# Performance work log

Hardware: AMD Instinct MI355X
Metric: run time of the kernel (lower is better)

Reference implementation:

```python
import jax, jax.numpy as jnp
import numpy as np

MAX_SX = 10  # max_shiftx
MAX_SY = 10  # max_shifty
STD_EPS = 1e-9


def setup_inputs() -> dict:
    key = jax.random.key(0)
    x = jax.random.normal(key, (8, 32, 128, 128), dtype=jnp.float32)
    return {"x": x}


def _cross_correlation(x):
    b, c, h, w = x.shape
    n = h * w
    # _standartize: zero-mean, divide by (unbiased std * sqrt(h*w)); std<eps -> inf -> 0
    xc = x - jnp.mean(x, axis=(2, 3), keepdims=True)
    std = jnp.std(xc, axis=(2, 3), keepdims=True, ddof=1)
    std = jnp.where(std < STD_EPS, jnp.inf, std)
    xs = xc / (std * jnp.sqrt(jnp.asarray(n, x.dtype)))
    # FFT-based circular cross-correlation for all ordered pairs (i, j>=i)
    Xf = jnp.fft.fft2(xs)  # [b, c, h, w] complex
    ii, jj = np.triu_indices(c)  # row-major: (0,0),(0,1),...,(0,c-1),(1,1),... matches the loop order
    cross = Xf[:, ii] * jnp.conj(Xf[:, jj])  # [b, P, h, w], P = c*(c+1)//2
    cc = jnp.real(jnp.fft.ifft2(cross))
    # The [[br, bl], [tr, tl]] corner concat == roll by (sy, sx) then take leading window
    cc = jnp.roll(cc, (MAX_SY, MAX_SX), axis=(2, 3))
    return cc[:, :, : 2 * MAX_SY + 1, : 2 * MAX_SX + 1]  # [b, P, 2sy+1, 2sx+1]


def reference(x):
    return _cross_correlation(x)
```

## Files before the change

### kernel.cpp

```cpp
#include <hip/hip_runtime.h>
#include <hip/hip_bf16.h>

typedef __attribute__((ext_vector_type(4))) unsigned int uint4v;
typedef __attribute__((ext_vector_type(8))) short short8;
typedef __attribute__((ext_vector_type(16))) float floatx16;

#define NROW 148
#define ROWB (20*512)
#define BB   ((size_t)NROW*ROWB)
#define STATS_OFF ((size_t)8*BB)
#define LDS_A_ROWS 38
#define LDS_BYTES (LDS_A_ROWS*2048 + 32*2048)

__device__ __forceinline__ unsigned short f2b(float f){
  unsigned int u = __float_as_uint(f);
  return (unsigned short)((u + 0x7fffu + ((u >> 16) & 1u)) >> 16);
}

__device__ __forceinline__ void gload_lds16(const void* g, void* l){
  __builtin_amdgcn_global_load_lds((const __attribute__((address_space(1))) unsigned int*)g,
                                   (__attribute__((address_space(3))) unsigned int*)l, 16, 0, 0);
}

__global__ __launch_bounds__(256) void k_stat(const float* __restrict__ x,
                                              float* __restrict__ stats){
  int bid = blockIdx.x;
  int t = threadIdx.x;
  const float* xc = x + ((size_t)bid << 14);
  float s = 0.f, ss = 0.f;
  #pragma unroll 4
  for (int k = 0; k < 64; ++k){
    float v = xc[t + (k << 8)];
    s += v; ss += v*v;
  }
  #pragma unroll
  for (int m = 32; m >= 1; m >>= 1){
    s  += __shfl_xor(s, m);
    ss += __shfl_xor(ss, m);
  }
  __shared__ float rs[4], rss[4];
  int wv = t >> 6, l = t & 63;
  if (l == 0){ rs[wv] = s; rss[wv] = ss; }
  __syncthreads();
  if (t == 0){
    float S  = rs[0]+rs[1]+rs[2]+rs[3];
    float SS = rss[0]+rss[1]+rss[2]+rss[3];
    float mean = S * (1.f/16384.f);
    float var  = (SS - S*mean) * (1.f/16383.f);
    float sd = sqrtf(fmaxf(var, 0.f));
    stats[bid*2]   = mean;
    stats[bid*2+1] = (sd < 1e-9f) ? 0.f : 1.f/(sd*128.f);
  }
}

__global__ __launch_bounds__(512) void k_pack(const float* __restrict__ x,
                                              const float* __restrict__ stats,
                                              unsigned char* __restrict__ pad){
  __shared__ float rowbuf[32*129];
  int bid = blockIdx.x;
  int b = bid & 7, rg = bid >> 3;
  int t = threadIdx.x;
  int ch = t >> 4, xq = t & 15;
  float mean  = stats[(b*32 + ch)*2];
  float scale = stats[(b*32 + ch)*2 + 1];
  const float* xc = x + ((size_t)(b*32 + ch) << 14);
  for (int rr = 0; rr < 4; ++rr){
    int r = rg*4 + rr;
    int sy = (r + 118) & 127;
    const float* src = xc + (sy << 7) + (xq << 3);
    float4 v0 = *(const float4*)src;
    float4 v1 = *(const float4*)(src + 4);
    float* rb = rowbuf + ch*129 + (xq << 3);
    rb[0] = (v0.x-mean)*scale; rb[1] = (v0.y-mean)*scale;
    rb[2] = (v0.z-mean)*scale; rb[3] = (v0.w-mean)*scale;
    rb[4] = (v1.x-mean)*scale; rb[5] = (v1.y-mean)*scale;
    rb[6] = (v1.z-mean)*scale; rb[7] = (v1.w-mean)*scale;
    __syncthreads();
    #pragma unroll
    for (int k = 0; k < 2; ++k){
      int q = t + (k << 9);
      if (q < 640){
        int col = q >> 5, cq = q & 31;
        const float* rbq = rowbuf + cq*129;
        unsigned int d[4];
        #pragma unroll
        for (int e = 0; e < 4; ++e){
          unsigned int lo = f2b(rbq[(8*col + 2*e)     & 127]);
          unsigned int hi = f2b(rbq[(8*col + 2*e + 1) & 127]);
          d[e] = lo | (hi << 16);
        }
        uint4v ov = {d[0], d[1], d[2], d[3]};
        *(uint4v*)(pad + ((size_t)(b*148 + r)*20 + col)*512 + cq*16) = ov;
      }
    }
    __syncthreads();
  }
}

#define WW(k3, idx) (aw[k3][(idx)>>2][(idx)&3])
#define SHIFT_STORE(OFS, ODD) \
  { _Pragma("unroll") \
    for (int k3 = 0; k3 < 3; ++k3){ \
      int pid = tid + (k3 << 9); \
      if (pid < 1216){ \
        char* dst = As + (pid >> 5)*2048 + (pid & 31)*16; \
        _Pragma("unroll") \
        for (int c = 0; c < 4; ++c){ \
          unsigned int o0,o1,o2,o3; \
          if (ODD){ \
            o0 = (WW(k3,4*c+OFS+0)>>16)|(WW(k3,4*c+OFS+1)<<16); \
            o1 = (WW(k3,4*c+OFS+1)>>16)|(WW(k3,4*c+OFS+2)<<16); \
            o2 = (WW(k3,4*c+OFS+2)>>16)|(WW(k3,4*c+OFS+3)<<16); \
            o3 = (WW(k3,4*c+OFS+3)>>16)|(WW(k3,4*c+OFS+4)<<16); \
          } else { \
            o0 = WW(k3,4*c+OFS+0); o1 = WW(k3,4*c+OFS+1); \
            o2 = WW(k3,4*c+OFS+2); o3 = WW(k3,4*c+OFS+3); \
          } \
          uint4v ov = {o0,o1,o2,o3}; \
          *(uint4v*)(dst + c*512) = ov; \
        } \
      } \
    } }

__global__ __launch_bounds__(512, 1) void k_corr(const unsigned char* __restrict__ pad,
                                                 float* __restrict__ out){
  extern __shared__ char lds[];
  char* As = lds;
  char* Bs = lds + LDS_A_ROWS*2048;
  float* sf = (float*)lds;

  int bid = blockIdx.x;
  int b = bid & 7, cg = bid >> 3;
  int dx, d0;
  if (cg < 2){ dx = 0; d0 = cg << 2; }
  else { int q = cg - 2; dx = 1 + q/3; d0 = -10 + 7*(q - 3*(q/3)); }
  int r2 = dx & 7, cwoff = dx >> 3;

  int tid = threadIdx.x;
  int lane = tid & 63, wvi = tid >> 6;
  int ks = wvi & 1, kq = wvi >> 1;
  unsigned offF = (unsigned)((2*ks + (lane >> 5))*512 + (lane & 31)*16);

  const unsigned char* pb = pad + (size_t)b*BB;

  floatx16 acc[7];
  #pragma unroll
  for (int d = 0; d < 7; ++d) acc[d] = (floatx16)(0.0f);

  uint4v aw[3][5];
  auto issueA = [&](int yi, int xi){
    int rab = 32*yi + 10 + d0;
    int cwb = 4*xi + cwoff;
    #pragma unroll
    for (int k3 = 0; k3 < 3; ++k3){
      int pid = tid + (k3 << 9);
      if (pid < 1216){
        const unsigned char* g = pb + ((size_t)((rab + (pid >> 5))*20 + cwb))*512 + (pid & 31)*16;
        #pragma unroll
        for (int kk = 0; kk < 5; ++kk)
          aw[k3][kk] = *(const uint4v*)(g + kk*512);
      }
    }
  };

  issueA(0, 0);

  for (int t = 0; t < 16; ++t){
    int yi = t >> 2, xi = t & 3;
    __syncthreads();
    int rbb = 32*yi + 10;
    #pragma unroll
    for (int k8 = 0; k8 < 8; ++k8){
      int idb = tid + (k8 << 9);
      const unsigned char* g = pb + ((size_t)((rbb + (idb >> 7))*20 + 4*xi + ((idb >> 5)&3)))*512 + (idb & 31)*16;
      gload_lds16(g, Bs + (unsigned)idb*16);
    }
    switch (r2){
      case 0: SHIFT_STORE(0, 0); break;
      case 1: SHIFT_STORE(0, 1); break;
      case 2: SHIFT_STORE(1, 0); break;
      case 3: SHIFT_STORE(1, 1); break;
      case 4: SHIFT_STORE(2, 0); break;
      case 5: SHIFT_STORE(2, 1); break;
      case 6: SHIFT_STORE(3, 0); break;
      case 7: SHIFT_STORE(3, 1); break;
    }
    __syncthreads();
    if (t < 15) issueA((t+1) >> 2, (t+1) & 3);
    const char* Ab = As + (kq*8)*2048 + offF;
    const char* Bb = Bs + (kq*8)*2048 + offF;
    short8 ring[8];
    #pragma unroll
    for (int w = 0; w < 7; ++w) ring[w] = *(const short8*)(Ab + w*2048);
    short8 bnxt = *(const short8*)Bb;
    __builtin_amdgcn_s_setprio(1);
    #pragma unroll
    for (int yl = 0; yl < 8; ++yl){
      short8 bf = bnxt;
      if (yl < 7){
        bnxt = *(const short8*)(Bb + (yl+1)*2048);
        ring[(yl+7)&7] = *(const short8*)(Ab + (yl+7)*2048);
      }
      #pragma unroll
      for (int d = 0; d < 7; ++d)
        acc[d] = __builtin_amdgcn_mfma_f32_32x32x16_bf16(ring[(yl+d)&7], bf, acc[d], 0, 0, 0);
    }
    __builtin_amdgcn_s_setprio(0);
  }

  __syncthreads();
  int baseb = b * 232848;
  #pragma unroll
  for (int d = 0; d < 7; ++d){
    #pragma unroll
    for (int r = 0; r < 16; ++r)
      sf[wvi*1024 + r*64 + lane] = acc[d][r];
    __syncthreads();
    int dy = d0 + d;
    #pragma unroll
    for (int k = 0; k < 2; ++k){
      int p = tid + (k << 9);
      float v = 0.f;
      #pragma unroll
      for (int w = 0; w < 8; ++w) v += sf[w*1024 + p];
      int reg = p >> 6, ln = p & 63;
      int i = (reg & 3) + 8*(reg >> 2) + 4*(ln >> 5);
      int j = ln & 31;
      if (i <= j){
        int pp = i*(65 - i)/2 + (j - i);
        out[baseb + pp*441 + (10+dy)*21 + (10+dx)] = v;
        if (i == j && (dy != 0 || dx != 0))
          out[baseb + pp*441 + (10-dy)*21 + (10-dx)] = v;
      } else {
        int pp = j*(65 - j)/2 + (i - j);
        out[baseb + pp*441 + (10-dy)*21 + (10-dx)] = v;
      }
    }
    __syncthreads();
  }
}

extern "C" void kernel_launch(void* const* d_in, const int* in_sizes, int n_in,
                              void* d_out, int out_size, void* d_ws, size_t ws_size,
                              hipStream_t stream){
  const float* x = (const float*)d_in[0];
  unsigned char* pad = (unsigned char*)d_ws;
  float* stats = (float*)((char*)d_ws + STATS_OFF);
  float* out = (float*)d_out;
  hipFuncSetAttribute((const void*)k_corr, hipFuncAttributeMaxDynamicSharedMemorySize,
                      LDS_BYTES);
  k_stat<<<dim3(256), dim3(256), 0, stream>>>(x, stats);
  k_pack<<<dim3(296), dim3(512), 0, stream>>>(x, stats, pad);
  k_corr<<<dim3(256), dim3(512), LDS_BYTES, stream>>>(pad, out);
}
```

Before: 86.77 us.

## Double-buffer shifted A tile in LDS and stream B operand from global

Drops the LDS staging of the B operand: each wave now loads its B fragments directly from global memory into registers through a 3-deep prefetch queue. The freed LDS holds a second A buffer, so the shifted A tile for the next step is written while the current one is consumed. This cuts the per-iteration barriers from two to one and pushes the A register prefetch two steps ahead. The cost is global-load latency sitting directly in the MFMA loop, and B data that several waves previously shared through LDS is now fetched redundantly from global or cache.

```diff
diff --git a/kernel.cpp b/kernel.cpp
--- a/kernel.cpp
+++ b/kernel.cpp
@@ -10,16 +10,12 @@
 #define BB   ((size_t)NROW*ROWB)
 #define STATS_OFF ((size_t)8*BB)
 #define LDS_A_ROWS 38
-#define LDS_BYTES (LDS_A_ROWS*2048 + 32*2048)
+#define ABUF (LDS_A_ROWS*2048)
+#define LDS_BYTES (2*ABUF)
 
 __device__ __forceinline__ unsigned short f2b(float f){
   unsigned int u = __float_as_uint(f);
   return (unsigned short)((u + 0x7fffu + ((u >> 16) & 1u)) >> 16);
-}
-
-__device__ __forceinline__ void gload_lds16(const void* g, void* l){
-  __builtin_amdgcn_global_load_lds((const __attribute__((address_space(1))) unsigned int*)g,
-                                   (__attribute__((address_space(3))) unsigned int*)l, 16, 0, 0);
 }
 
 __global__ __launch_bounds__(256) void k_stat(const float* __restrict__ x,
@@ -103,7 +99,7 @@
     for (int k3 = 0; k3 < 3; ++k3){ \
       int pid = tid + (k3 << 9); \
       if (pid < 1216){ \
-        char* dst = As + (pid >> 5)*2048 + (pid & 31)*16; \
+        char* dst = Asw + (pid >> 5)*2048 + (pid & 31)*16; \
         _Pragma("unroll") \
         for (int c = 0; c < 4; ++c){ \
           unsigned int o0,o1,o2,o3; \
@@ -121,12 +117,22 @@
         } \
       } \
     } }
+#define DO_SHIFT_STORE() \
+  switch (r2){ \
+    case 0: SHIFT_STORE(0, 0); break; \
+    case 1: SHIFT_STORE(0, 1); break; \
+    case 2: SHIFT_STORE(1, 0); break; \
+    case 3: SHIFT_STORE(1, 1); break; \
+    case 4: SHIFT_STORE(2, 0); break; \
+    case 5: SHIFT_STORE(2, 1); break; \
+    case 6: SHIFT_STORE(3, 0); break; \
+    case 7: SHIFT_STORE(3, 1); break; \
+  }
 
 __global__ __launch_bounds__(512, 1) void k_corr(const unsigned char* __restrict__ pad,
                                                  float* __restrict__ out){
   extern __shared__ char lds[];
   char* As = lds;
-  char* Bs = lds + LDS_A_ROWS*2048;
   float* sf = (float*)lds;
 
   int bid = blockIdx.x;
@@ -148,9 +154,9 @@
   for (int d = 0; d < 7; ++d) acc[d] = (floatx16)(0.0f);
 
   uint4v aw[3][5];
-  auto issueA = [&](int yi, int xi){
-    int rab = 32*yi + 10 + d0;
-    int cwb = 4*xi + cwoff;
+  auto issueA = [&](int tt){
+    int rab = 32*(tt >> 2) + 10 + d0;
+    int cwb = 4*(tt & 3) + cwoff;
     #pragma unroll
     for (int k3 = 0; k3 < 3; ++k3){
       int pid = tid + (k3 << 9);
@@ -163,52 +169,37 @@
     }
   };
 
-  issueA(0, 0);
+  issueA(0);
+  { char* Asw = As; DO_SHIFT_STORE(); }
+  issueA(1);
+  __syncthreads();
 
   for (int t = 0; t < 16; ++t){
-    int yi = t >> 2, xi = t & 3;
-    __syncthreads();
-    int rbb = 32*yi + 10;
-    #pragma unroll
-    for (int k8 = 0; k8 < 8; ++k8){
-      int idb = tid + (k8 << 9);
-      const unsigned char* g = pb + ((size_t)((rbb + (idb >> 7))*20 + 4*xi + ((idb >> 5)&3)))*512 + (idb & 31)*16;
-      gload_lds16(g, Bs + (unsigned)idb*16);
-    }
-    switch (r2){
-      case 0: SHIFT_STORE(0, 0); break;
-      case 1: SHIFT_STORE(0, 1); break;
-      case 2: SHIFT_STORE(1, 0); break;
-      case 3: SHIFT_STORE(1, 1); break;
-      case 4: SHIFT_STORE(2, 0); break;
-      case 5: SHIFT_STORE(2, 1); break;
-      case 6: SHIFT_STORE(3, 0); break;
-      case 7: SHIFT_STORE(3, 1); break;
-    }
-    __syncthreads();
-    if (t < 15) issueA((t+1) >> 2, (t+1) & 3);
-    const char* Ab = As + (kq*8)*2048 + offF;
-    const char* Bb = Bs + (kq*8)*2048 + offF;
+    if (t < 15){ char* Asw = As + ((t+1)&1)*ABUF; DO_SHIFT_STORE(); }
+    if (t < 14) issueA(t+2);
+    const char* Ab = As + (t&1)*ABUF + (kq*8)*2048 + offF;
+    const unsigned char* pBw = pb + ((size_t)((32*(t>>2) + 10 + kq*8)*20 + 4*(t&3) + 2*ks))*512
+                               + (unsigned)((lane >> 5)*512 + (lane & 31)*16);
     short8 ring[8];
     #pragma unroll
     for (int w = 0; w < 7; ++w) ring[w] = *(const short8*)(Ab + w*2048);
-    short8 bnxt = *(const short8*)Bb;
+    short8 BQ[3];
+    #pragma unroll
+    for (int k = 0; k < 3; ++k) BQ[k] = *(const short8*)(pBw + (size_t)k*ROWB);
     __builtin_amdgcn_s_setprio(1);
     #pragma unroll
     for (int yl = 0; yl < 8; ++yl){
-      short8 bf = bnxt;
-      if (yl < 7){
-        bnxt = *(const short8*)(Bb + (yl+1)*2048);
-        ring[(yl+7)&7] = *(const short8*)(Ab + (yl+7)*2048);
-      }
+      short8 bf = BQ[yl % 3];
+      if (yl < 5) BQ[yl % 3] = *(const short8*)(pBw + (size_t)(yl + 3)*ROWB);
+      if (yl < 7) ring[(yl+7)&7] = *(const short8*)(Ab + (yl+7)*2048);
       #pragma unroll
       for (int d = 0; d < 7; ++d)
         acc[d] = __builtin_amdgcn_mfma_f32_32x32x16_bf16(ring[(yl+d)&7], bf, acc[d], 0, 0, 0);
     }
     __builtin_amdgcn_s_setprio(0);
-  }
-
-  __syncthreads();
+    __syncthreads();
+  }
+
   int baseb = b * 232848;
   #pragma unroll
   for (int d = 0; d < 7; ++d){
```

New measurement: 81.04 us. -6.6%, faster.
